# Performance work log

Measured on AMD Instinct MI355X. Metric: run time of the kernel, lower is better.

The kernel has to match this reference:

```python
import jax, jax.numpy as jnp
import numpy as np

B = 1024
P = 8
D = 2048
NUM_IDS = 64
MARGIN = 0.3
EPS = 1e-12


def setup_inputs() -> dict:
    key = jax.random.key(0)
    k1, k2, k3 = jax.random.split(key, 3)
    feats = jax.random.normal(k1, (B, P * D), dtype=jnp.float32)
    labels = jax.random.randint(k2, (B,), 0, NUM_IDS, dtype=jnp.int64)
    subs = jax.random.randint(k3, (B,), 0, 2, dtype=jnp.int64)
    return {"feats": feats, "labels": labels, "subs": subs}


def reference(feats, labels, subs):
    b = feats.shape[0]
    f = feats.reshape(b, -1, D)  # [B, P, D]
    dt = f.dtype

    # Per-sample class centers via a single segment-mean pass
    # (equivalent to the original per-sample boolean-mask mean loop).
    seg_sum = jax.ops.segment_sum(f, labels, num_segments=NUM_IDS)  # [NUM_IDS, P, D]
    counts = jax.ops.segment_sum(jnp.ones((b,), dt), labels, num_segments=NUM_IDS)
    centers_by_id = seg_sum / jnp.maximum(counts, 1.0)[:, None, None]
    centers = centers_by_id[labels]  # [B, P, D]

    # dist_ap[i] = sum_p ||f[i,p] - center[i,p]||
    d_ap = jnp.sqrt(jnp.clip(jnp.sum((f - centers) ** 2, axis=-1), EPS, None)).sum(-1)  # [B]
    dist_ap = d_ap[:, None] + d_ap[None, :]  # [B, B]

    # pairwise_distance: dist_aa[i,j] = sum_p ||f[i,p] - f[j,p]||, via gemm trick
    sq = jnp.sum(f * f, axis=-1)  # [B, P]
    inner = jnp.einsum('ipd,jpd->ijp', f, f)  # [B, B, P]
    d2 = sq[:, None, :] + sq[None, :, :] - 2.0 * inner
    dist_aa = jnp.sqrt(jnp.clip(d2, EPS, None)).sum(-1)  # [B, B]

    # masked margin loss over negative (different-label) pairs
    mask = labels[:, None] != labels[None, :]  # [B, B] bool
    vals = jnp.clip(dist_ap - dist_aa + MARGIN, 0.0, None)
    maskf = mask.astype(dt)
    loss = jnp.sum(vals * maskf) / jnp.sum(maskf)
    return loss
```

## Files before the change

### kernel.cpp

```cpp
#include <hip/hip_runtime.h>
#include <hip/hip_bf16.h>

#define B_ 1024
#define P_ 8
#define D_ 2048
#define FD_ (P_ * D_)
#define NID 64
#define MARGIN_ 0.3f
#define EPS_ 1e-12f

typedef unsigned short u16;
typedef float float4_t __attribute__((ext_vector_type(4)));

#define AS1 __attribute__((address_space(1)))
#define AS3 __attribute__((address_space(3)))

__device__ __forceinline__ float bf2f(unsigned v) {
    unsigned x = v << 16;
    float f;
    __builtin_memcpy(&f, &x, 4);
    return f;
}

static const size_t OFF_COUNTS = 0;
static const size_t OFF_OFFS   = 256;
static const size_t OFF_PERM   = 512;
static const size_t OFF_NEG    = 4608;
static const size_t OFF_POS    = 8176;
static const size_t OFF_S      = 8192;
static const size_t OFF_SQ     = 40960;
static const size_t OFF_DAP    = 73728;
static const size_t OFF_FB     = 131072;
static const size_t OFF_PD     = OFF_FB + (size_t)B_ * FD_;

__global__ void k_counts(const int* __restrict__ labels, float* countsf, int* offs,
                         int* perm, float* negcnt) {
    __shared__ int h[NID], o[NID], cur[NID];
    int tid = threadIdx.x;
    if (tid < NID) h[tid] = 0;
    __syncthreads();
    for (int i = tid; i < B_; i += 256) atomicAdd(&h[labels[i]], 1);
    __syncthreads();
    if (tid == 0) {
        int acc = 0;
        long long ss = 0;
        for (int c = 0; c < NID; c++) {
            o[c] = acc;
            acc += h[c];
            ss += (long long)h[c] * h[c];
        }
        *negcnt = (float)((long long)B_ * B_ - ss);
    }
    __syncthreads();
    if (tid < NID) {
        countsf[tid] = (float)h[tid];
        offs[tid] = o[tid];
        cur[tid] = o[tid];
    }
    __syncthreads();
    for (int i = tid; i < B_; i += 256) {
        int pos = atomicAdd(&cur[labels[i]], 1);
        perm[pos] = i;
    }
}

__global__ void k_rowstats(const float* __restrict__ feats, unsigned char* __restrict__ fb,
                           float* __restrict__ sq) {
    int i = blockIdx.x;
    int tid = threadIdx.x;
    int p = tid >> 6, lane = tid & 63;
    const float* frow = feats + (size_t)i * FD_ + p * D_;
    unsigned char* brow = fb + (size_t)p * B_ * D_ + (size_t)i * D_;
    float s2 = 0.f;
#pragma unroll
    for (int ch = 0; ch < 8; ch++) {
        int d = ch * 256 + lane * 4;
        float4 f = *(const float4*)(frow + d);
        int pk = __builtin_amdgcn_cvt_pk_fp8_f32(f.x, f.y, 0, false);
        pk = __builtin_amdgcn_cvt_pk_fp8_f32(f.z, f.w, pk, true);
        *(unsigned int*)(brow + d) = (unsigned int)pk;
        s2 += f.x * f.x + f.y * f.y + f.z * f.z + f.w * f.w;
    }
    for (int o = 32; o; o >>= 1) s2 += __shfl_down(s2, o, 64);
    if (lane == 0) sq[i * P_ + p] = s2;
}

__global__ __launch_bounds__(256, 4) void k_pairs(const unsigned char* __restrict__ fb,
                                                  const float* __restrict__ sq,
                                                  const int* __restrict__ labels,
                                                  float* __restrict__ S,
                                                  u16* __restrict__ pd) {
    const int p  = blockIdx.x;
    const int j0 = blockIdx.y * 128;
    const int i0 = blockIdx.z * 128;
    __shared__ __align__(16) unsigned char As[16384];
    __shared__ __align__(16) unsigned char Bs[16384];
    __shared__ float sqAs[128], sqBs[128];
    __shared__ int labA[128], labB[128];
    const int tid = threadIdx.x;
    const int lane = tid & 63, wid = tid >> 6;
    if (tid < 128) {
        sqAs[tid] = sq[(i0 + tid) * 8 + p];
        labA[tid] = labels[i0 + tid];
    } else {
        int t = tid - 128;
        sqBs[t] = sq[(j0 + t) * 8 + p];
        labB[t] = labels[j0 + t];
    }

    const int wi = (wid >> 1) * 64, wj = (wid & 1) * 64;
    const int lhi = lane >> 4, llo = lane & 15;
    const int sl = llo & 7;
    const int lr = lane >> 3;
    const int lc = (lane & 7) ^ lr;

    const size_t plbase = (size_t)p * ((size_t)B_ * D_);
    const unsigned char* gA[4];
    const unsigned char* gB[4];
    unsigned char* lA[4];
    unsigned char* lB[4];
#pragma unroll
    for (int inst = 0; inst < 4; inst++) {
        int r0 = wid * 32 + inst * 8;
        gA[inst] = fb + plbase + (size_t)(i0 + r0 + lr) * D_ + lc * 16;
        gB[inst] = fb + plbase + (size_t)(j0 + r0 + lr) * D_ + lc * 16;
        lA[inst] = As + r0 * 128;
        lB[inst] = Bs + r0 * 128;
    }

    float4_t acc[4][4];
#pragma unroll
    for (int a = 0; a < 4; a++)
#pragma unroll
        for (int b = 0; b < 4; b++) acc[a][b] = (float4_t){0.f, 0.f, 0.f, 0.f};

    for (int kb = 0; kb < 16; kb++) {
        const int koff = kb * 128;
        __syncthreads();
#pragma unroll
        for (int inst = 0; inst < 4; inst++) {
            __builtin_amdgcn_global_load_lds((const AS1 void*)(gA[inst] + koff),
                                             (AS3 void*)lA[inst], 16, 0, 0);
            __builtin_amdgcn_global_load_lds((const AS1 void*)(gB[inst] + koff),
                                             (AS3 void*)lB[inst], 16, 0, 0);
        }
        __syncthreads();
#pragma unroll
        for (int ks = 0; ks < 4; ks++) {
            const int pcb = ((2 * ks + (lhi >> 1)) ^ sl) * 16 + (lhi & 1) * 8;
            long af[4], bf[4];
#pragma unroll
            for (int a = 0; a < 4; a++) {
                af[a] = *(const long*)(As + (wi + a * 16 + llo) * 128 + pcb);
                bf[a] = *(const long*)(Bs + (wj + a * 16 + llo) * 128 + pcb);
            }
#pragma unroll
            for (int a = 0; a < 4; a++)
#pragma unroll
                for (int b = 0; b < 4; b++)
                    acc[a][b] = __builtin_amdgcn_mfma_f32_16x16x32_fp8_fp8(
                        af[a], bf[b], acc[a][b], 0, 0, 0);
        }
    }
    u16* outp = pd + (size_t)p * B_ * B_;
    float rs[4][4];
#pragma unroll
    for (int a = 0; a < 4; a++)
#pragma unroll
        for (int r = 0; r < 4; r++) rs[a][r] = 0.f;
#pragma unroll
    for (int a = 0; a < 4; a++) {
        int la0 = labA[wi + a * 16 + lhi * 4 + 0];
        int la1 = labA[wi + a * 16 + lhi * 4 + 1];
        int la2 = labA[wi + a * 16 + lhi * 4 + 2];
        int la3 = labA[wi + a * 16 + lhi * 4 + 3];
#pragma unroll
        for (int b = 0; b < 4; b++) {
            int jl = wj + b * 16 + llo;
            int lb = labB[jl];
#pragma unroll
            for (int r = 0; r < 4; r++) {
                int il = wi + a * 16 + lhi * 4 + r;
                float t = acc[a][b][r];
                float d2 = sqAs[il] + sqBs[jl] - 2.0f * t;
                outp[(size_t)(i0 + il) * B_ + (j0 + jl)] =
                    __bfloat16_as_ushort(__float2bfloat16(sqrtf(fmaxf(d2, EPS_))));
                int la = (r == 0) ? la0 : (r == 1) ? la1 : (r == 2) ? la2 : la3;
                if (lb == la) rs[a][r] += t;
            }
        }
    }
#pragma unroll
    for (int a = 0; a < 4; a++)
#pragma unroll
        for (int r = 0; r < 4; r++) {
            float v = rs[a][r];
            v += __shfl_xor(v, 1, 64);
            v += __shfl_xor(v, 2, 64);
            v += __shfl_xor(v, 4, 64);
            v += __shfl_xor(v, 8, 64);
            if (llo == 0)
                atomicAdd(&S[(size_t)(i0 + wi + a * 16 + lhi * 4 + r) * 8 + p], v);
        }
}

__global__ void k_dap(const float* __restrict__ S, const float* __restrict__ sq,
                      const float* __restrict__ countsf, const int* __restrict__ offs,
                      const int* __restrict__ perm, float* __restrict__ dap) {
    int c = blockIdx.x;
    int tid = threadIdx.x;
    int cnt = (int)countsf[c];
    int off = offs[c];
    __shared__ float T[8];
    if (tid < 8) {
        float t = 0.f;
        for (int m = 0; m < cnt; m++) t += S[(size_t)perm[off + m] * 8 + tid];
        T[tid] = t;
    }
    __syncthreads();
    float n = fmaxf((float)cnt, 1.f);
    float inv = 1.f / n, inv2 = inv * inv;
    for (int m = tid; m < cnt; m += 64) {
        int i = perm[off + m];
        float d = 0.f;
#pragma unroll
        for (int p = 0; p < 8; p++) {
            float d2 = sq[i * 8 + p] - 2.f * inv * S[(size_t)i * 8 + p] + inv2 * T[p];
            d += sqrtf(fmaxf(d2, EPS_));
        }
        dap[i] = d;
    }
}

__global__ void k_lossred(const u16* __restrict__ pd, const float* __restrict__ dap,
                          const int* __restrict__ labels, float* possum) {
    int i = blockIdx.x;
    int tid = threadIdx.x;
    float di = dap[i];
    int li = labels[i];
    int jb = tid * 4;
    float daa0 = 0.f, daa1 = 0.f, daa2 = 0.f, daa3 = 0.f;
#pragma unroll
    for (int p = 0; p < 8; p++) {
        uint2 v = *(const uint2*)&pd[((size_t)p << 20) + (size_t)i * B_ + jb];
        daa0 += bf2f(v.x & 0xFFFFu);
        daa1 += bf2f(v.x >> 16);
        daa2 += bf2f(v.y & 0xFFFFu);
        daa3 += bf2f(v.y >> 16);
    }
    float lsum = 0.f;
    float daas[4] = {daa0, daa1, daa2, daa3};
#pragma unroll
    for (int q = 0; q < 4; q++) {
        int j = jb + q;
        if (labels[j] != li) lsum += fmaxf(di + dap[j] - daas[q] + MARGIN_, 0.f);
    }
    for (int o = 32; o; o >>= 1) lsum += __shfl_down(lsum, o, 64);
    __shared__ float red[4];
    int wid = tid >> 6, lane = tid & 63;
    if (lane == 0) red[wid] = lsum;
    __syncthreads();
    if (tid == 0) atomicAdd(possum, red[0] + red[1] + red[2] + red[3]);
}

__global__ void k_finalize(const float* possum, const float* negcnt, float* out) {
    out[0] = possum[0] / negcnt[0];
}

extern "C" void kernel_launch(void* const* d_in, const int* in_sizes, int n_in,
                              void* d_out, int out_size, void* d_ws, size_t ws_size,
                              hipStream_t stream) {
    const float* feats = (const float*)d_in[0];
    const int* labels  = (const int*)d_in[1];
    float* out = (float*)d_out;

    char* w = (char*)d_ws;
    float* countsf = (float*)(w + OFF_COUNTS);
    int* offs      = (int*)(w + OFF_OFFS);
    int* perm      = (int*)(w + OFF_PERM);
    float* negcnt  = (float*)(w + OFF_NEG);
    float* possum  = (float*)(w + OFF_POS);
    float* S       = (float*)(w + OFF_S);
    float* sq      = (float*)(w + OFF_SQ);
    float* dap     = (float*)(w + OFF_DAP);
    unsigned char* fb = (unsigned char*)(w + OFF_FB);
    u16* pd        = (u16*)(w + OFF_PD);

    hipMemsetAsync(w + OFF_POS, 0, (OFF_S - OFF_POS) + (size_t)B_ * P_ * 4, stream);

    k_counts<<<1, 256, 0, stream>>>(labels, countsf, offs, perm, negcnt);
    k_rowstats<<<B_, 512, 0, stream>>>(feats, fb, sq);
    k_pairs<<<dim3(8, 8, 8), 256, 0, stream>>>(fb, sq, labels, S, pd);
    k_dap<<<NID, 64, 0, stream>>>(S, sq, countsf, offs, perm, dap);
    k_lossred<<<B_, 256, 0, stream>>>(pd, dap, labels, possum);
    k_finalize<<<1, 1, 0, stream>>>(possum, negcnt, out);
}
```

Before: 174.5 us.

## Split GEMM K dimension across two wave groups and fuse small kernels

The pairwise fp8 GEMM block grows to 512 threads. Two groups of four waves each take half of the D dimension, and their partial accumulators are combined through LDS before the epilogue. This doubles the waves per block and so adds latency hiding, at the cost of 64KB of LDS per block, an extra LDS round trip, and an epilogue where half the waves sit idle. The label-count kernel is merged into the rowstats kernel as one extra block. The finalize kernel is replaced by a last-block ticket inside the loss reduction, which removes two launches.

After: 181.9 us. +4.2%, slower.

```diff
diff --git a/kernel.cpp b/kernel.cpp
--- a/kernel.cpp
+++ b/kernel.cpp
@@ -26,66 +26,66 @@
 static const size_t OFF_OFFS   = 256;
 static const size_t OFF_PERM   = 512;
 static const size_t OFF_NEG    = 4608;
-static const size_t OFF_POS    = 8176;
+static const size_t OFF_POS    = 8168;
+static const size_t OFF_TICKET = 8172;
 static const size_t OFF_S      = 8192;
 static const size_t OFF_SQ     = 40960;
 static const size_t OFF_DAP    = 73728;
 static const size_t OFF_FB     = 131072;
 static const size_t OFF_PD     = OFF_FB + (size_t)B_ * FD_;
 
-__global__ void k_counts(const int* __restrict__ labels, float* countsf, int* offs,
-                         int* perm, float* negcnt) {
-    __shared__ int h[NID], o[NID], cur[NID];
+__global__ void k_prep(const float* __restrict__ feats, const int* __restrict__ labels,
+                       unsigned char* __restrict__ fb, float* __restrict__ sq,
+                       float* countsf, int* offs, int* perm, float* negcnt) {
     int tid = threadIdx.x;
-    if (tid < NID) h[tid] = 0;
-    __syncthreads();
-    for (int i = tid; i < B_; i += 256) atomicAdd(&h[labels[i]], 1);
-    __syncthreads();
-    if (tid == 0) {
-        int acc = 0;
-        long long ss = 0;
-        for (int c = 0; c < NID; c++) {
-            o[c] = acc;
-            acc += h[c];
-            ss += (long long)h[c] * h[c];
-        }
-        *negcnt = (float)((long long)B_ * B_ - ss);
-    }
-    __syncthreads();
-    if (tid < NID) {
-        countsf[tid] = (float)h[tid];
-        offs[tid] = o[tid];
-        cur[tid] = o[tid];
-    }
-    __syncthreads();
-    for (int i = tid; i < B_; i += 256) {
-        int pos = atomicAdd(&cur[labels[i]], 1);
-        perm[pos] = i;
-    }
-}
-
-__global__ void k_rowstats(const float* __restrict__ feats, unsigned char* __restrict__ fb,
-                           float* __restrict__ sq) {
-    int i = blockIdx.x;
-    int tid = threadIdx.x;
-    int p = tid >> 6, lane = tid & 63;
-    const float* frow = feats + (size_t)i * FD_ + p * D_;
-    unsigned char* brow = fb + (size_t)p * B_ * D_ + (size_t)i * D_;
-    float s2 = 0.f;
-#pragma unroll
-    for (int ch = 0; ch < 8; ch++) {
-        int d = ch * 256 + lane * 4;
-        float4 f = *(const float4*)(frow + d);
-        int pk = __builtin_amdgcn_cvt_pk_fp8_f32(f.x, f.y, 0, false);
-        pk = __builtin_amdgcn_cvt_pk_fp8_f32(f.z, f.w, pk, true);
-        *(unsigned int*)(brow + d) = (unsigned int)pk;
-        s2 += f.x * f.x + f.y * f.y + f.z * f.z + f.w * f.w;
-    }
-    for (int o = 32; o; o >>= 1) s2 += __shfl_down(s2, o, 64);
-    if (lane == 0) sq[i * P_ + p] = s2;
-}
-
-__global__ __launch_bounds__(256, 4) void k_pairs(const unsigned char* __restrict__ fb,
+    if (blockIdx.x < B_) {
+        int i = blockIdx.x;
+        int p = tid >> 6, lane = tid & 63;
+        const float* frow = feats + (size_t)i * FD_ + p * D_;
+        unsigned char* brow = fb + (size_t)p * B_ * D_ + (size_t)i * D_;
+        float s2 = 0.f;
+#pragma unroll
+        for (int ch = 0; ch < 8; ch++) {
+            int d = ch * 256 + lane * 4;
+            float4 f = *(const float4*)(frow + d);
+            int pk = __builtin_amdgcn_cvt_pk_fp8_f32(f.x, f.y, 0, false);
+            pk = __builtin_amdgcn_cvt_pk_fp8_f32(f.z, f.w, pk, true);
+            *(unsigned int*)(brow + d) = (unsigned int)pk;
+            s2 += f.x * f.x + f.y * f.y + f.z * f.z + f.w * f.w;
+        }
+        for (int o = 32; o; o >>= 1) s2 += __shfl_down(s2, o, 64);
+        if (lane == 0) sq[i * P_ + p] = s2;
+    } else {
+        __shared__ int h[NID], o[NID], cur[NID];
+        if (tid < NID) h[tid] = 0;
+        __syncthreads();
+        for (int i = tid; i < B_; i += 512) atomicAdd(&h[labels[i]], 1);
+        __syncthreads();
+        if (tid == 0) {
+            int acc = 0;
+            long long ss = 0;
+            for (int c = 0; c < NID; c++) {
+                o[c] = acc;
+                acc += h[c];
+                ss += (long long)h[c] * h[c];
+            }
+            *negcnt = (float)((long long)B_ * B_ - ss);
+        }
+        __syncthreads();
+        if (tid < NID) {
+            countsf[tid] = (float)h[tid];
+            offs[tid] = o[tid];
+            cur[tid] = o[tid];
+        }
+        __syncthreads();
+        for (int i = tid; i < B_; i += 512) {
+            int pos = atomicAdd(&cur[labels[i]], 1);
+            perm[pos] = i;
+        }
+    }
+}
+
+__global__ __launch_bounds__(512, 4) void k_pairs(const unsigned char* __restrict__ fb,
                                                   const float* __restrict__ sq,
                                                   const int* __restrict__ labels,
                                                   float* __restrict__ S,
@@ -93,37 +93,41 @@
     const int p  = blockIdx.x;
     const int j0 = blockIdx.y * 128;
     const int i0 = blockIdx.z * 128;
-    __shared__ __align__(16) unsigned char As[16384];
-    __shared__ __align__(16) unsigned char Bs[16384];
+    __shared__ __align__(16) unsigned char smem[65536];
     __shared__ float sqAs[128], sqBs[128];
     __shared__ int labA[128], labB[128];
     const int tid = threadIdx.x;
     const int lane = tid & 63, wid = tid >> 6;
+    const int s = wid & 3, h = wid >> 2;
     if (tid < 128) {
         sqAs[tid] = sq[(i0 + tid) * 8 + p];
         labA[tid] = labels[i0 + tid];
-    } else {
+    } else if (tid < 256) {
         int t = tid - 128;
         sqBs[t] = sq[(j0 + t) * 8 + p];
         labB[t] = labels[j0 + t];
     }
 
-    const int wi = (wid >> 1) * 64, wj = (wid & 1) * 64;
+    const int wi = (s >> 1) * 64, wj = (s & 1) * 64;
     const int lhi = lane >> 4, llo = lane & 15;
     const int sl = llo & 7;
     const int lr = lane >> 3;
     const int lc = (lane & 7) ^ lr;
 
+    unsigned char* const As = smem + h * 16384;
+    unsigned char* const Bs = smem + 32768 + h * 16384;
+
     const size_t plbase = (size_t)p * ((size_t)B_ * D_);
+    const size_t colbase = (size_t)h * 1024 + (size_t)lc * 16;
     const unsigned char* gA[4];
     const unsigned char* gB[4];
     unsigned char* lA[4];
     unsigned char* lB[4];
 #pragma unroll
     for (int inst = 0; inst < 4; inst++) {
-        int r0 = wid * 32 + inst * 8;
-        gA[inst] = fb + plbase + (size_t)(i0 + r0 + lr) * D_ + lc * 16;
-        gB[inst] = fb + plbase + (size_t)(j0 + r0 + lr) * D_ + lc * 16;
+        int r0 = s * 32 + inst * 8;
+        gA[inst] = fb + plbase + (size_t)(i0 + r0 + lr) * D_ + colbase;
+        gB[inst] = fb + plbase + (size_t)(j0 + r0 + lr) * D_ + colbase;
         lA[inst] = As + r0 * 128;
         lB[inst] = Bs + r0 * 128;
     }
@@ -134,7 +138,7 @@
 #pragma unroll
         for (int b = 0; b < 4; b++) acc[a][b] = (float4_t){0.f, 0.f, 0.f, 0.f};
 
-    for (int kb = 0; kb < 16; kb++) {
+    for (int kb = 0; kb < 8; kb++) {
         const int koff = kb * 128;
         __syncthreads();
 #pragma unroll
@@ -162,46 +166,59 @@
                         af[a], bf[b], acc[a][b], 0, 0, 0);
         }
     }
-    u16* outp = pd + (size_t)p * B_ * B_;
-    float rs[4][4];
-#pragma unroll
-    for (int a = 0; a < 4; a++)
-#pragma unroll
-        for (int r = 0; r < 4; r++) rs[a][r] = 0.f;
-#pragma unroll
-    for (int a = 0; a < 4; a++) {
-        int la0 = labA[wi + a * 16 + lhi * 4 + 0];
-        int la1 = labA[wi + a * 16 + lhi * 4 + 1];
-        int la2 = labA[wi + a * 16 + lhi * 4 + 2];
-        int la3 = labA[wi + a * 16 + lhi * 4 + 3];
-#pragma unroll
-        for (int b = 0; b < 4; b++) {
-            int jl = wj + b * 16 + llo;
-            int lb = labB[jl];
+    __syncthreads();
+    float* ep = (float*)smem;
+    if (h == 1) {
+#pragma unroll
+        for (int a = 0; a < 4; a++)
+#pragma unroll
+            for (int b = 0; b < 4; b++)
+                *(float4_t*)&ep[(((s * 4 + a) * 4 + b) * 64 + lane) * 4] = acc[a][b];
+    }
+    __syncthreads();
+    if (h == 0) {
+        u16* outp = pd + (size_t)p * B_ * B_;
+        float rs[4][4];
+#pragma unroll
+        for (int a = 0; a < 4; a++)
+#pragma unroll
+            for (int r = 0; r < 4; r++) rs[a][r] = 0.f;
+#pragma unroll
+        for (int a = 0; a < 4; a++) {
+            int la0 = labA[wi + a * 16 + lhi * 4 + 0];
+            int la1 = labA[wi + a * 16 + lhi * 4 + 1];
+            int la2 = labA[wi + a * 16 + lhi * 4 + 2];
+            int la3 = labA[wi + a * 16 + lhi * 4 + 3];
+#pragma unroll
+            for (int b = 0; b < 4; b++) {
+                float4_t o = *(const float4_t*)&ep[(((s * 4 + a) * 4 + b) * 64 + lane) * 4];
+                int jl = wj + b * 16 + llo;
+                int lb = labB[jl];
+#pragma unroll
+                for (int r = 0; r < 4; r++) {
+                    int il = wi + a * 16 + lhi * 4 + r;
+                    float t = acc[a][b][r] + o[r];
+                    float d2 = sqAs[il] + sqBs[jl] - 2.0f * t;
+                    outp[(size_t)(i0 + il) * B_ + (j0 + jl)] =
+                        __bfloat16_as_ushort(__float2bfloat16(sqrtf(fmaxf(d2, EPS_))));
+                    int la = (r == 0) ? la0 : (r == 1) ? la1 : (r == 2) ? la2 : la3;
+                    if (lb == la) rs[a][r] += t;
+                }
+            }
+        }
+#pragma unroll
+        for (int a = 0; a < 4; a++)
 #pragma unroll
             for (int r = 0; r < 4; r++) {
-                int il = wi + a * 16 + lhi * 4 + r;
-                float t = acc[a][b][r];
-                float d2 = sqAs[il] + sqBs[jl] - 2.0f * t;
-                outp[(size_t)(i0 + il) * B_ + (j0 + jl)] =
-                    __bfloat16_as_ushort(__float2bfloat16(sqrtf(fmaxf(d2, EPS_))));
-                int la = (r == 0) ? la0 : (r == 1) ? la1 : (r == 2) ? la2 : la3;
-                if (lb == la) rs[a][r] += t;
+                float v = rs[a][r];
+                v += __shfl_xor(v, 1, 64);
+                v += __shfl_xor(v, 2, 64);
+                v += __shfl_xor(v, 4, 64);
+                v += __shfl_xor(v, 8, 64);
+                if (llo == 0)
+                    atomicAdd(&S[(size_t)(i0 + wi + a * 16 + lhi * 4 + r) * 8 + p], v);
             }
-        }
-    }
-#pragma unroll
-    for (int a = 0; a < 4; a++)
-#pragma unroll
-        for (int r = 0; r < 4; r++) {
-            float v = rs[a][r];
-            v += __shfl_xor(v, 1, 64);
-            v += __shfl_xor(v, 2, 64);
-            v += __shfl_xor(v, 4, 64);
-            v += __shfl_xor(v, 8, 64);
-            if (llo == 0)
-                atomicAdd(&S[(size_t)(i0 + wi + a * 16 + lhi * 4 + r) * 8 + p], v);
-        }
+    }
 }
 
 __global__ void k_dap(const float* __restrict__ S, const float* __restrict__ sq,
@@ -233,7 +250,8 @@
 }
 
 __global__ void k_lossred(const u16* __restrict__ pd, const float* __restrict__ dap,
-                          const int* __restrict__ labels, float* possum) {
+                          const int* __restrict__ labels, float* possum,
+                          const float* negcnt, int* ticket, float* out) {
     int i = blockIdx.x;
     int tid = threadIdx.x;
     float di = dap[i];
@@ -260,11 +278,15 @@
     int wid = tid >> 6, lane = tid & 63;
     if (lane == 0) red[wid] = lsum;
     __syncthreads();
-    if (tid == 0) atomicAdd(possum, red[0] + red[1] + red[2] + red[3]);
-}
-
-__global__ void k_finalize(const float* possum, const float* negcnt, float* out) {
-    out[0] = possum[0] / negcnt[0];
+    if (tid == 0) {
+        atomicAdd(possum, red[0] + red[1] + red[2] + red[3]);
+        __threadfence();
+        int t = atomicAdd(ticket, 1);
+        if (t == B_ - 1) {
+            float total = atomicAdd(possum, 0.0f);
+            out[0] = total / negcnt[0];
+        }
+    }
 }
 
 extern "C" void kernel_launch(void* const* d_in, const int* in_sizes, int n_in,
@@ -280,6 +302,7 @@
     int* perm      = (int*)(w + OFF_PERM);
     float* negcnt  = (float*)(w + OFF_NEG);
     float* possum  = (float*)(w + OFF_POS);
+    int* ticket    = (int*)(w + OFF_TICKET);
     float* S       = (float*)(w + OFF_S);
     float* sq      = (float*)(w + OFF_SQ);
     float* dap     = (float*)(w + OFF_DAP);
@@ -288,10 +311,8 @@
 
     hipMemsetAsync(w + OFF_POS, 0, (OFF_S - OFF_POS) + (size_t)B_ * P_ * 4, stream);
 
-    k_counts<<<1, 256, 0, stream>>>(labels, countsf, offs, perm, negcnt);
-    k_rowstats<<<B_, 512, 0, stream>>>(feats, fb, sq);
-    k_pairs<<<dim3(8, 8, 8), 256, 0, stream>>>(fb, sq, labels, S, pd);
+    k_prep<<<B_ + 1, 512, 0, stream>>>(feats, labels, fb, sq, countsf, offs, perm, negcnt);
+    k_pairs<<<dim3(8, 8, 8), 512, 0, stream>>>(fb, sq, labels, S, pd);
     k_dap<<<NID, 64, 0, stream>>>(S, sq, countsf, offs, perm, dap);
-    k_lossred<<<B_, 256, 0, stream>>>(pd, dap, labels, possum);
-    k_finalize<<<1, 1, 0, stream>>>(possum, negcnt, out);
-}
+    k_lossred<<<B_, 256, 0, stream>>>(pd, dap, labels, possum, negcnt, ticket, out);
+}
```
